# Performance work log

Hardware: AMD Instinct MI355X
Metric: run time of the kernel (lower is better)

The kernel has to match this reference:

```python
import jax, jax.numpy as jnp
import numpy as np

N = 32768      # nodes
DIN = 256      # in_channels (space dim; hyperbolic input has DIN+1 dims)
DOUT = 256     # out_channels
H = 8          # num_heads
K = 1.0        # Lorentz curvature manifold.k
P = 2          # power_k
EPS = 1e-6


def _lorentz(key, n, d):
    # random point on Lorentz manifold: time = sqrt(||space||^2 + k)
    s = jax.random.normal(key, (n, d), jnp.float32)
    t = jnp.sqrt(jnp.sum(s * s, -1, keepdims=True) + K)
    return jnp.concatenate([t, s], -1)


def setup_inputs() -> dict:
    key = jax.random.key(0)
    ks = jax.random.split(key, 8)
    sc = 0.02
    return {
        "query_input": _lorentz(ks[0], N, DIN),
        "source_input": _lorentz(ks[1], N, DIN),
        "Wq_w": jax.random.normal(ks[2], (H, DOUT, DIN + 1), jnp.float32) * sc,
        "Wq_b": jnp.zeros((H, DOUT), jnp.float32),
        "Wk_w": jax.random.normal(ks[3], (H, DOUT, DIN + 1), jnp.float32) * sc,
        "Wk_b": jnp.zeros((H, DOUT), jnp.float32),
        "Wv_w": jax.random.normal(ks[4], (H, DOUT, DIN + 1), jnp.float32) * sc,
        "Wv_b": jnp.zeros((H, DOUT), jnp.float32),
        "norm_scale": jnp.ones((), jnp.float32),
        "v_map_w": jax.random.normal(ks[5], (DOUT, DIN), jnp.float32) * sc,
        "v_map_b": jnp.zeros((DOUT,), jnp.float32),
        "final_w": jax.random.normal(ks[6], (DOUT, H * DOUT), jnp.float32) * sc,
        "final_b": jnp.zeros((DOUT,), jnp.float32),
    }


def _hyp_linear(x, W, b):
    # HypLinear for all heads at once. x: [N, Din+1], W: [H, Dout, Din+1], b: [H, Dout]
    xs = jnp.einsum('ni,hoi->nho', x, W) + b              # space part [N,H,Dout]
    xt = jnp.sqrt(jnp.sum(xs * xs, -1, keepdims=True) + K)  # Lorentz time
    return jnp.concatenate([xt, xs], -1)                  # [N,H,Dout+1]


def _fp(x, p=P):
    # fp(x) = ||x|| / ||x^p|| * x^p  (per-vector rescaled power map)
    norm_x = jnp.linalg.norm(x, axis=-1, keepdims=True)
    xp = x ** p
    norm_xp = jnp.linalg.norm(xp, axis=-1, keepdims=True)
    return norm_x / norm_xp * xp


def reference(query_input, source_input, Wq_w, Wq_b, Wk_w, Wk_b, Wv_w, Wv_b,
              norm_scale, v_map_w, v_map_b, final_w, final_b):
    q = _hyp_linear(query_input, Wq_w, Wq_b)    # [N,H,D+1]
    k = _hyp_linear(source_input, Wk_w, Wk_b)   # [N,H,D+1]
    v = _hyp_linear(source_input, Wv_w, Wv_b)   # [N,H,D+1]

    # linear_focus_attention: drop time dim
    qs, ks_, vs = q[..., 1:], k[..., 1:], v[..., 1:]     # [N,H,D]
    dscale = jnp.abs(norm_scale) + EPS
    phi_q = _fp((jax.nn.relu(qs) + EPS) / dscale)
    phi_k = _fp((jax.nn.relu(ks_) + EPS) / dscale)

    ktv = jnp.einsum('nhm,nhd->hmd', phi_k, vs)          # [H,D,D]
    numerator = jnp.einsum('nhm,hmd->nhd', phi_q, ktv)   # [N,H,D]
    denominator = jnp.einsum('nhd,hd->nh', phi_q, jnp.sum(phi_k, 0))[..., None]
    attn = numerator / (denominator + EPS)

    vss = vs @ v_map_w.T + v_map_b                       # v_map_mlp(v)
    attn = attn + vss

    # trans_heads_concat -> final_linear
    out = attn.reshape(N, H * DOUT) @ final_w.T + final_b  # [N,Dout]

    # lift back to Lorentz manifold
    t = jnp.sqrt(jnp.sum(out * out, -1, keepdims=True) + K)
    return jnp.concatenate([t, out], -1)                 # [N,Dout+1]
```

## Files before the change

kernel.cpp:

```cpp
#include <hip/hip_runtime.h>
#include <hip/hip_bf16.h>


#define EPSF 1e-6f

typedef __attribute__((ext_vector_type(8))) short bf16x8;
typedef __attribute__((ext_vector_type(8))) unsigned short u16x8;
typedef __attribute__((ext_vector_type(4))) float f32x4;
typedef float f32x4a __attribute__((ext_vector_type(4), aligned(4)));

__device__ __forceinline__ float b2f(unsigned short u) {
    union { unsigned int i; float f; } c;
    c.i = ((unsigned int)u) << 16;
    return c.f;
}
__device__ __forceinline__ unsigned short f2b(float f) {
    __hip_bfloat16 h = __float2bfloat16(f);
    union { __hip_bfloat16 h; unsigned short u; } c;
    c.h = h;
    return c.u;
}

__global__ void zero_kernel(float* __restrict__ p, int n) {
    int i = blockIdx.x * 256 + threadIdx.x;
    if (i < n) p[i] = 0.f;
}

__global__ __launch_bounds__(256) void wconv_kernel(
    const float* __restrict__ Wq, const float* __restrict__ Wk, const float* __restrict__ Wv,
    const float* __restrict__ Bq, const float* __restrict__ Bk, const float* __restrict__ Bv,
    unsigned short* __restrict__ Wbf, float* __restrict__ biasAll)
{
    const int t = threadIdx.x;
    const int b = blockIdx.x;
    if (b < 6144) {
        const int mat = b >> 11, lr = b & 2047;
        const float* Ws = (mat == 0 ? Wq : mat == 1 ? Wk : Wv) + (size_t)lr * 257;
        Wbf[(size_t)b * 288 + t] = f2b(Ws[t]);
        if (t < 32) {
            float v = (t == 0) ? Ws[256] : 0.f;
            Wbf[(size_t)b * 288 + 256 + t] = f2b(v);
        }
    } else {
        const int e = (b - 6144) * 256 + t;
        const int mat = e >> 11, r = e & 2047;
        biasAll[e] = (mat == 0 ? Bq : mat == 1 ? Bk : Bv)[r];
    }
}

__global__ __launch_bounds__(256) void w2g_kernel(
    const float* __restrict__ vmw,
    const float* __restrict__ fw,
    float* __restrict__ G32)
{
    const int t = threadIdx.x;
    const int h = blockIdx.x >> 3;
    const int i0 = (blockIdx.x & 7) * 32;

    __shared__ __align__(16) float xlds[16][40];
    __shared__ float wlds[256][17];

    float acc[32];
#pragma unroll
    for (int r = 0; r < 32; ++r) acc[r] = 0.f;

    const int ar = t >> 3;
    const int ak = (t & 7) * 2;
    const int wk = t & 15;
    const int wo = (t >> 4) * 16;

    for (int d0 = 0; d0 < 256; d0 += 16) {
        xlds[ak][ar]     = vmw[(size_t)(d0 + ak) * 256 + i0 + ar];
        xlds[ak + 1][ar] = vmw[(size_t)(d0 + ak + 1) * 256 + i0 + ar];
#pragma unroll
        for (int j = 0; j < 16; ++j)
            wlds[wo + j][wk] = fw[(size_t)(wo + j) * 2048 + h * 256 + d0 + wk];
        __syncthreads();
#pragma unroll
        for (int kk = 0; kk < 16; ++kk) {
            float bv = wlds[t][kk];
            const float4* xr = (const float4*)(&xlds[kk][0]);
#pragma unroll
            for (int g = 0; g < 8; ++g) {
                float4 xv = xr[g];
                acc[g * 4 + 0] = fmaf(xv.x, bv, acc[g * 4 + 0]);
                acc[g * 4 + 1] = fmaf(xv.y, bv, acc[g * 4 + 1]);
                acc[g * 4 + 2] = fmaf(xv.z, bv, acc[g * 4 + 2]);
                acc[g * 4 + 3] = fmaf(xv.w, bv, acc[g * 4 + 3]);
            }
        }
        __syncthreads();
    }
#pragma unroll
    for (int r = 0; r < 32; ++r)
        G32[(size_t)t * 2048 + h * 256 + i0 + r] = acc[r];
}

__global__ __launch_bounds__(256) void bias2_kernel(
    const float* __restrict__ vmb, const float* __restrict__ fw,
    const float* __restrict__ fb, const float* __restrict__ Bv,
    const float* __restrict__ G32, float* __restrict__ bias2)
{
    const int o = blockIdx.x;
    const int t = threadIdx.x;
    float s = 0.f, sb = 0.f;
#pragma unroll
    for (int i = 0; i < 8; ++i) {
        const int j = t + i * 256;
        s += fw[(size_t)o * 2048 + j];
        sb += Bv[j] * G32[(size_t)o * 2048 + j];
    }
    s = s * vmb[t] + sb;
#pragma unroll
    for (int off = 32; off > 0; off >>= 1) s += __shfl_down(s, off, 64);
    __shared__ float r4[4];
    if ((t & 63) == 0) r4[t >> 6] = s;
    __syncthreads();
    if (t == 0) bias2[o] = fb[o] + r4[0] + r4[1] + r4[2] + r4[3];
}

__global__ __launch_bounds__(256) void gm_kernel(
    const float* __restrict__ Wv, const float* __restrict__ G32,
    float* __restrict__ Mf32)
{
    __shared__ float Gt[64][33];
    __shared__ float Wt[32][33];
    const int t = threadIdx.x;
    const int o0 = blockIdx.x * 64, i0 = blockIdx.y * 32, k0 = blockIdx.z * 256;
    const int ii = t & 31, og = t >> 5;
    float acc[8] = {};
    for (int kk0 = k0; kk0 < k0 + 256; kk0 += 32) {
#pragma unroll
        for (int r = 0; r < 8; ++r) {
            const int e = t + r * 256;
            Gt[e >> 5][e & 31] = G32[(size_t)(o0 + (e >> 5)) * 2048 + kk0 + (e & 31)];
        }
#pragma unroll
        for (int r = 0; r < 4; ++r) {
            const int e = t + r * 256;
            const int kk = e >> 5, i = i0 + (e & 31);
            Wt[kk][e & 31] = (i < 257) ? Wv[(size_t)(kk0 + kk) * 257 + i] : 0.f;
        }
        __syncthreads();
#pragma unroll
        for (int kk = 0; kk < 32; ++kk) {
            float wv_ = Wt[kk][ii];
#pragma unroll
            for (int r = 0; r < 8; ++r)
                acc[r] = fmaf(Gt[og * 8 + r][kk], wv_, acc[r]);
        }
        __syncthreads();
    }
#pragma unroll
    for (int r = 0; r < 8; ++r)
        atomicAdd(&Mf32[(size_t)(o0 + og * 8 + r) * 288 + i0 + ii], acc[r]);
}

__global__ void gmcvt_kernel(const float* __restrict__ Mf32, unsigned short* __restrict__ Mbf) {
    const int i = blockIdx.x * 256 + threadIdx.x;
    Mbf[i] = f2b(Mf32[i]);
}

__global__ __launch_bounds__(256) void proj_mfma(
    const float* __restrict__ X,
    const unsigned short* __restrict__ Wbase,
    const float* __restrict__ biasBase,
    unsigned short* __restrict__ outT,
    int CH)
{
    __shared__ __align__(16) unsigned short smem[10240];
    __shared__ float rowx[128];
    unsigned short* lA = smem;
    unsigned short* lB = smem + 128 * 40;
    const int t = threadIdx.x;
    const int m0 = blockIdx.x * 128;
    const int c0 = blockIdx.y * 128;
    const int lane = t & 63, w = t >> 6;
    const int wm = (w >> 1) * 64, wn = (w & 1) * 64;
    const int l15 = lane & 15, q = lane >> 4;
    const int ar = t >> 2, akg = (t & 3) * 8;

    f32x4 acc[4][4] = {};
    const float* XA = X + (size_t)(m0 + ar) * 257 + akg;
    const unsigned short* WB = Wbase + (size_t)(c0 + ar) * 288 + akg;

    f32x4a cx[2][2];
    u16x8 cw[2];
#pragma unroll
    for (int qq = 0; qq < 2; ++qq) {
        cx[qq][0] = *(const f32x4a*)(XA + (size_t)qq * 64 * 257);
        cx[qq][1] = *(const f32x4a*)(XA + (size_t)qq * 64 * 257 + 4);
        cw[qq]    = *(const u16x8*)(WB + (size_t)qq * 64 * 288);
    }

    for (int ks = 0; ks < 8; ++ks) {
#pragma unroll
        for (int qq = 0; qq < 2; ++qq) {
            u16x8 pk;
            pk[0] = f2b(cx[qq][0][0]); pk[1] = f2b(cx[qq][0][1]);
            pk[2] = f2b(cx[qq][0][2]); pk[3] = f2b(cx[qq][0][3]);
            pk[4] = f2b(cx[qq][1][0]); pk[5] = f2b(cx[qq][1][1]);
            pk[6] = f2b(cx[qq][1][2]); pk[7] = f2b(cx[qq][1][3]);
            *(u16x8*)(&lA[(ar + qq * 64) * 40 + akg]) = pk;
            *(u16x8*)(&lB[(ar + qq * 64) * 40 + akg]) = cw[qq];
        }
        if (ks < 7) {
            const int k1 = (ks + 1) * 32;
#pragma unroll
            for (int qq = 0; qq < 2; ++qq) {
                cx[qq][0] = *(const f32x4a*)(XA + (size_t)qq * 64 * 257 + k1);
                cx[qq][1] = *(const f32x4a*)(XA + (size_t)qq * 64 * 257 + k1 + 4);
                cw[qq]    = *(const u16x8*)(WB + (size_t)qq * 64 * 288 + k1);
            }
        }
        __syncthreads();
        bf16x8 af[4], bfr[4];
#pragma unroll
        for (int i = 0; i < 4; ++i)
            af[i] = *(const bf16x8*)(&lA[(wm + i * 16 + l15) * 40 + q * 8]);
#pragma unroll
        for (int j = 0; j < 4; ++j)
            bfr[j] = *(const bf16x8*)(&lB[(wn + j * 16 + l15) * 40 + q * 8]);
#pragma unroll
        for (int i = 0; i < 4; ++i)
#pragma unroll
            for (int j = 0; j < 4; ++j)
                acc[i][j] = __builtin_amdgcn_mfma_f32_16x16x32_bf16(af[i], bfr[j], acc[i][j], 0, 0, 0);
        __syncthreads();
    }

    if (t < 128) rowx[t] = b2f(f2b(X[(size_t)(m0 + t) * 257 + 256]));
    __syncthreads();

#pragma unroll
    for (int j = 0; j < 4; ++j) {
        const int cg = c0 + wn + j * 16 + l15;
        const float w256 = b2f(Wbase[(size_t)cg * 288 + 256]);
        const float bias = biasBase[cg];
#pragma unroll
        for (int i = 0; i < 4; ++i)
#pragma unroll
            for (int r = 0; r < 4; ++r)
                acc[i][j][r] += rowx[wm + i * 16 + q * 4 + r] * w256 + bias;
    }

#pragma unroll
    for (int p = 0; p < 2; ++p) {
        __syncthreads();
        if ((w >> 1) == p) {
#pragma unroll
            for (int i = 0; i < 4; ++i)
#pragma unroll
                for (int j = 0; j < 4; ++j) {
                    const int cl = wn + j * 16 + l15;
#pragma unroll
                    for (int r2 = 0; r2 < 4; r2 += 2) {
                        const int nl = i * 16 + q * 4 + r2;
                        const unsigned int pk =
                            (unsigned int)f2b(acc[i][j][r2]) |
                            ((unsigned int)f2b(acc[i][j][r2 + 1]) << 16);
                        *(unsigned int*)(&smem[cl * 64 + (((nl >> 3) ^ (cl & 7)) << 3) + (nl & 7)]) = pk;
                    }
                }
        }
        __syncthreads();
#pragma unroll
        for (int k = 0; k < 4; ++k) {
            const int task = k * 256 + t;
            const int cl = task >> 3, nq = task & 7;
            *(u16x8*)(outT + (size_t)(c0 + cl) * CH + m0 + p * 64 + nq * 8) =
                *(const u16x8*)(&smem[cl * 64 + ((nq ^ (cl & 7)) << 3)]);
        }
    }
}

__global__ __launch_bounds__(256) void xm_mfma(
    const float* __restrict__ X,
    const unsigned short* __restrict__ Mbf,
    float* __restrict__ outp)
{
    __shared__ __align__(16) unsigned short smem[10240];
    __shared__ float rowx[128];
    unsigned short* lA = smem;
    unsigned short* lB = smem + 128 * 40;
    const int t = threadIdx.x;
    const int m0 = blockIdx.x * 128;
    const int c0 = blockIdx.y * 128;
    const int lane = t & 63, w = t >> 6;
    const int wm = (w >> 1) * 64, wn = (w & 1) * 64;
    const int l15 = lane & 15, q = lane >> 4;
    const int ar = t >> 2, akg = (t & 3) * 8;

    f32x4 acc[4][4] = {};
    const float* XA = X + (size_t)(m0 + ar) * 257 + akg;
    const unsigned short* WB = Mbf + (size_t)(c0 + ar) * 288 + akg;

    f32x4a cx[2][2];
    u16x8 cw[2];
#pragma unroll
    for (int qq = 0; qq < 2; ++qq) {
        cx[qq][0] = *(const f32x4a*)(XA + (size_t)qq * 64 * 257);
        cx[qq][1] = *(const f32x4a*)(XA + (size_t)qq * 64 * 257 + 4);
        cw[qq]    = *(const u16x8*)(WB + (size_t)qq * 64 * 288);
    }

    for (int ks = 0; ks < 8; ++ks) {
#pragma unroll
        for (int qq = 0; qq < 2; ++qq) {
            u16x8 pk;
            pk[0] = f2b(cx[qq][0][0]); pk[1] = f2b(cx[qq][0][1]);
            pk[2] = f2b(cx[qq][0][2]); pk[3] = f2b(cx[qq][0][3]);
            pk[4] = f2b(cx[qq][1][0]); pk[5] = f2b(cx[qq][1][1]);
            pk[6] = f2b(cx[qq][1][2]); pk[7] = f2b(cx[qq][1][3]);
            *(u16x8*)(&lA[(ar + qq * 64) * 40 + akg]) = pk;
            *(u16x8*)(&lB[(ar + qq * 64) * 40 + akg]) = cw[qq];
        }
        if (ks < 7) {
            const int k1 = (ks + 1) * 32;
#pragma unroll
            for (int qq = 0; qq < 2; ++qq) {
                cx[qq][0] = *(const f32x4a*)(XA + (size_t)qq * 64 * 257 + k1);
                cx[qq][1] = *(const f32x4a*)(XA + (size_t)qq * 64 * 257 + k1 + 4);
                cw[qq]    = *(const u16x8*)(WB + (size_t)qq * 64 * 288 + k1);
            }
        }
        __syncthreads();
        bf16x8 af[4], bfr[4];
#pragma unroll
        for (int i = 0; i < 4; ++i)
            af[i] = *(const bf16x8*)(&lA[(wm + i * 16 + l15) * 40 + q * 8]);
#pragma unroll
        for (int j = 0; j < 4; ++j)
            bfr[j] = *(const bf16x8*)(&lB[(wn + j * 16 + l15) * 40 + q * 8]);
#pragma unroll
        for (int i = 0; i < 4; ++i)
#pragma unroll
            for (int j = 0; j < 4; ++j)
                acc[i][j] = __builtin_amdgcn_mfma_f32_16x16x32_bf16(af[i], bfr[j], acc[i][j], 0, 0, 0);
        __syncthreads();
    }

    if (t < 128) rowx[t] = b2f(f2b(X[(size_t)(m0 + t) * 257 + 256]));
    __syncthreads();

#pragma unroll
    for (int j = 0; j < 4; ++j) {
        const int cg = c0 + wn + j * 16 + l15;
        const float w256 = b2f(Mbf[(size_t)cg * 288 + 256]);
#pragma unroll
        for (int i = 0; i < 4; ++i)
#pragma unroll
            for (int r = 0; r < 4; ++r) {
                const int n = m0 + wm + i * 16 + q * 4 + r;
                outp[(size_t)n * 257 + 1 + cg] =
                    acc[i][j][r] + rowx[wm + i * 16 + q * 4 + r] * w256;
            }
    }
}

__global__ __launch_bounds__(256) void proj_phi(
    const float* __restrict__ X,
    const unsigned short* __restrict__ Wbase,
    const float* __restrict__ biasBase,
    unsigned short* __restrict__ outbuf,
    const float* __restrict__ nsc,
    const float* __restrict__ colsum_in,
    float* __restrict__ colsum_rep,
    int mode, int CH)
{
    __shared__ __align__(16) unsigned short smem[16384];
    __shared__ float reds2[4][64];
    __shared__ float reds4[4][64];
    __shared__ float rowv[64];
    __shared__ float rowx[64];
    unsigned short* lA = smem;
    unsigned short* lB = smem + 64 * 40;

    const int t = threadIdx.x;
    const int m0 = blockIdx.x * 64;
    const int h  = blockIdx.y;
    const int lane = t & 63, w = t >> 6;
    const int wn = w * 64;
    const int l15 = lane & 15, q = lane >> 4;
    const int ar = t >> 2, akg = (t & 3) * 8;

    f32x4 acc[4][4] = {};
    const float* XA = X + (size_t)(m0 + ar) * 257 + akg;
    const unsigned short* WB = Wbase + (size_t)(h * 256 + ar) * 288 + akg;

    f32x4a cx0, cx1;
    u16x8 cw[4];
    cx0 = *(const f32x4a*)(XA);
    cx1 = *(const f32x4a*)(XA + 4);
#pragma unroll
    for (int qq = 0; qq < 4; ++qq)
        cw[qq] = *(const u16x8*)(WB + (size_t)qq * 64 * 288);

    for (int ks = 0; ks < 8; ++ks) {
        {
            u16x8 pk;
            pk[0] = f2b(cx0[0]); pk[1] = f2b(cx0[1]);
            pk[2] = f2b(cx0[2]); pk[3] = f2b(cx0[3]);
            pk[4] = f2b(cx1[0]); pk[5] = f2b(cx1[1]);
            pk[6] = f2b(cx1[2]); pk[7] = f2b(cx1[3]);
            *(u16x8*)(&lA[ar * 40 + akg]) = pk;
        }
#pragma unroll
        for (int qq = 0; qq < 4; ++qq)
            *(u16x8*)(&lB[(ar + qq * 64) * 40 + akg]) = cw[qq];
        if (ks < 7) {
            const int k1 = (ks + 1) * 32;
            cx0 = *(const f32x4a*)(XA + k1);
            cx1 = *(const f32x4a*)(XA + k1 + 4);
#pragma unroll
            for (int qq = 0; qq < 4; ++qq)
                cw[qq] = *(const u16x8*)(WB + (size_t)qq * 64 * 288 + k1);
        }
        __syncthreads();
        bf16x8 af[4], bfr[4];
#pragma unroll
        for (int i = 0; i < 4; ++i)
            af[i] = *(const bf16x8*)(&lA[(i * 16 + l15) * 40 + q * 8]);
#pragma unroll
        for (int j = 0; j < 4; ++j)
            bfr[j] = *(const bf16x8*)(&lB[(wn + j * 16 + l15) * 40 + q * 8]);
#pragma unroll
        for (int i = 0; i < 4; ++i)
#pragma unroll
            for (int j = 0; j < 4; ++j)
                acc[i][j] = __builtin_amdgcn_mfma_f32_16x16x32_bf16(af[i], bfr[j], acc[i][j], 0, 0, 0);
        __syncthreads();
    }

    if (t < 64) rowx[t] = b2f(f2b(X[(size_t)(m0 + t) * 257 + 256]));
    __syncthreads();

    {
        float w256[4];
#pragma unroll
        for (int j = 0; j < 4; ++j)
            w256[j] = b2f(Wbase[(size_t)(h * 256 + wn + j * 16 + l15) * 288 + 256]);
#pragma unroll
        for (int i = 0; i < 4; ++i)
#pragma unroll
            for (int r = 0; r < 4; ++r) {
                const float xv = rowx[i * 16 + q * 4 + r];
#pragma unroll
                for (int j = 0; j < 4; ++j)
                    acc[i][j][r] += xv * w256[j];
            }
    }

    const float c = fabsf(nsc[0]) + EPSF;
    float bias[4];
#pragma unroll
    for (int j = 0; j < 4; ++j) bias[j] = biasBase[h * 256 + wn + j * 16 + l15];

    float a2[4][4], a4[4][4];
#pragma unroll
    for (int i = 0; i < 4; ++i)
#pragma unroll
        for (int r = 0; r < 4; ++r) { a2[i][r] = 0.f; a4[i][r] = 0.f; }
#pragma unroll
    for (int i = 0; i < 4; ++i)
#pragma unroll
        for (int j = 0; j < 4; ++j)
#pragma unroll
            for (int r = 0; r < 4; ++r) {
                float uu = fmaxf(acc[i][j][r] + bias[j], 0.f) + EPSF;
                float q2 = uu * uu;
                acc[i][j][r] = q2;
                a2[i][r] += q2;
                a4[i][r] += q2 * q2;
            }
#pragma unroll
    for (int m = 1; m <= 8; m <<= 1) {
#pragma unroll
        for (int i = 0; i < 4; ++i)
#pragma unroll
            for (int r = 0; r < 4; ++r) {
                a2[i][r] += __shfl_xor(a2[i][r], m, 64);
                a4[i][r] += __shfl_xor(a4[i][r], m, 64);
            }
    }
    if (l15 == 0) {
#pragma unroll
        for (int i = 0; i < 4; ++i)
#pragma unroll
            for (int r = 0; r < 4; ++r) {
                reds2[w][i * 16 + q * 4 + r] = a2[i][r];
                reds4[w][i * 16 + q * 4 + r] = a4[i][r];
            }
    }
    __syncthreads();
    if (t < 64) {
        float s2t = reds2[0][t] + reds2[1][t] + reds2[2][t] + reds2[3][t];
        float s4t = reds4[0][t] + reds4[1][t] + reds4[2][t] + reds4[3][t];
        rowv[t] = sqrtf(s2t) / (c * sqrtf(s4t));
    }
    __syncthreads();
    float sc_[4][4];
#pragma unroll
    for (int i = 0; i < 4; ++i)
#pragma unroll
        for (int r = 0; r < 4; ++r) sc_[i][r] = rowv[i * 16 + q * 4 + r];

    if (mode == 0) {
        float colp[4];
#pragma unroll
        for (int j = 0; j < 4; ++j) colp[j] = 0.f;
#pragma unroll
        for (int i = 0; i < 4; ++i)
#pragma unroll
            for (int j = 0; j < 4; ++j)
#pragma unroll
                for (int r = 0; r < 4; ++r) {
                    float ph = acc[i][j][r] * sc_[i][r];
                    acc[i][j][r] = ph;
                    colp[j] += ph;
                }
#pragma unroll
        for (int i = 0; i < 4; ++i)
#pragma unroll
            for (int j = 0; j < 4; ++j) {
                const int cl = wn + j * 16 + l15;
#pragma unroll
                for (int r2 = 0; r2 < 4; r2 += 2) {
                    const int nl = i * 16 + q * 4 + r2;
                    const unsigned int pk =
                        (unsigned int)f2b(acc[i][j][r2]) |
                        ((unsigned int)f2b(acc[i][j][r2 + 1]) << 16);
                    *(unsigned int*)(&smem[cl * 64 + (((nl >> 3) ^ (cl & 7)) << 3) + (nl & 7)]) = pk;
                }
            }
        __syncthreads();
#pragma unroll
        for (int k = 0; k < 8; ++k) {
            const int task = k * 256 + t;
            const int cl = task >> 3, nq = task & 7;
            *(u16x8*)(outbuf + (size_t)(h * 256 + cl) * CH + m0 + nq * 8) =
                *(const u16x8*)(&smem[cl * 64 + ((nq ^ (cl & 7)) << 3)]);
        }
#pragma unroll
        for (int j = 0; j < 4; ++j) {
            colp[j] += __shfl_xor(colp[j], 16, 64);
            colp[j] += __shfl_xor(colp[j], 32, 64);
        }
        if (q == 0) {
            float* dst = colsum_rep + (size_t)(blockIdx.x & 7) * 2048;
#pragma unroll
            for (int j = 0; j < 4; ++j)
                atomicAdd(&dst[h * 256 + wn + j * 16 + l15], colp[j]);
        }
    } else {
        float cs[4];
#pragma unroll
        for (int j = 0; j < 4; ++j) cs[j] = colsum_in[h * 256 + wn + j * 16 + l15];
        float dp[4][4];
#pragma unroll
        for (int i = 0; i < 4; ++i)
#pragma unroll
            for (int r = 0; r < 4; ++r) dp[i][r] = 0.f;
#pragma unroll
        for (int i = 0; i < 4; ++i)
#pragma unroll
            for (int j = 0; j < 4; ++j)
#pragma unroll
                for (int r = 0; r < 4; ++r) {
                    float ph = acc[i][j][r] * sc_[i][r];
                    acc[i][j][r] = ph;
                    dp[i][r] += ph * cs[j];
                }
#pragma unroll
        for (int m = 1; m <= 8; m <<= 1) {
#pragma unroll
            for (int i = 0; i < 4; ++i)
#pragma unroll
                for (int r = 0; r < 4; ++r)
                    dp[i][r] += __shfl_xor(dp[i][r], m, 64);
        }
        if (l15 == 0) {
#pragma unroll
            for (int i = 0; i < 4; ++i)
#pragma unroll
                for (int r = 0; r < 4; ++r)
                    reds2[w][i * 16 + q * 4 + r] = dp[i][r];
        }
        __syncthreads();
        if (t < 64) {
            float dt = reds2[0][t] + reds2[1][t] + reds2[2][t] + reds2[3][t];
            rowv[t] = 1.f / (dt + EPSF);
        }
        __syncthreads();
#pragma unroll
        for (int i = 0; i < 4; ++i)
#pragma unroll
            for (int r = 0; r < 4; ++r) sc_[i][r] = rowv[i * 16 + q * 4 + r];
#pragma unroll
        for (int i = 0; i < 4; ++i)
#pragma unroll
            for (int j = 0; j < 4; ++j)
#pragma unroll
                for (int r = 0; r < 4; ++r) {
                    const int n = m0 + i * 16 + q * 4 + r;
                    outbuf[(size_t)n * 2048 + h * 256 + wn + j * 16 + l15] =
                        f2b(acc[i][j][r] * sc_[i][r]);
                }
    }
}

__global__ __launch_bounds__(256) void merge_colsum(
    const float* __restrict__ rep, float* __restrict__ out)
{
    const int cidx = blockIdx.x * 256 + threadIdx.x;
    float s = 0.f;
#pragma unroll
    for (int r = 0; r < 8; ++r) s += rep[(size_t)r * 2048 + cidx];
    out[cidx] = s;
}

__global__ __launch_bounds__(256) void ktv_mfma(
    const unsigned short* __restrict__ phiT,
    const unsigned short* __restrict__ vsT,
    float* __restrict__ ktv, int CH)
{
    __shared__ __align__(16) unsigned short lAT[128 * 64];
    __shared__ __align__(16) unsigned short lBT[128 * 64];
    const int t = threadIdx.x;
    const int h = blockIdx.y;
    const int split = blockIdx.x >> 2;
    const int tile = blockIdx.x & 3;
    const int m0 = (tile >> 1) * 128, d0 = (tile & 1) * 128;
    const int chh = h * 256;
    const int lane = t & 63, w = t >> 6;
    const int wm = (w >> 1) * 64, wn = (w & 1) * 64;
    const int l15 = lane & 15, q = lane >> 4;
    const int sl7 = l15 & 7;

    const int scg  = t >> 3;
    const int snq  = t & 7;
    const int sbase = scg * 64 + ((snq ^ (scg & 7)) << 3);

    f32x4 acc[4][4] = {};
    const int nb0 = split * 512;

    const unsigned short* pA = phiT + (size_t)(chh + m0 + scg) * CH + snq * 8;
    const unsigned short* pB = vsT  + (size_t)(chh + d0 + scg) * CH + snq * 8;

    u16x8 cA[4], cB[4], nA[4], nB[4];
#pragma unroll
    for (int k = 0; k < 4; ++k) {
        cA[k] = *(const u16x8*)(pA + (size_t)(k * 32) * CH + nb0);
        cB[k] = *(const u16x8*)(pB + (size_t)(k * 32) * CH + nb0);
    }

    for (int it = 0; it < 8; ++it) {
#pragma unroll
        for (int k = 0; k < 4; ++k) {
            *(u16x8*)(&lAT[k * 2048 + sbase]) = cA[k];
            *(u16x8*)(&lBT[k * 2048 + sbase]) = cB[k];
        }
        if (it < 7) {
            const int nb = nb0 + (it + 1) * 64;
#pragma unroll
            for (int k = 0; k < 4; ++k) {
                nA[k] = *(const u16x8*)(pA + (size_t)(k * 32) * CH + nb);
                nB[k] = *(const u16x8*)(pB + (size_t)(k * 32) * CH + nb);
            }
        }
        __syncthreads();
#pragma unroll
        for (int sub = 0; sub < 2; ++sub) {
            const int slot = ((sub * 4 + q) ^ sl7) << 3;
            bf16x8 af[4], bfr[4];
#pragma unroll
            for (int i = 0; i < 4; ++i)
                af[i] = *(const bf16x8*)(&lAT[(wm + i * 16 + l15) * 64 + slot]);
#pragma unroll
            for (int j = 0; j < 4; ++j)
                bfr[j] = *(const bf16x8*)(&lBT[(wn + j * 16 + l15) * 64 + slot]);
#pragma unroll
            for (int i = 0; i < 4; ++i)
#pragma unroll
                for (int j = 0; j < 4; ++j)
                    acc[i][j] = __builtin_amdgcn_mfma_f32_16x16x32_bf16(af[i], bfr[j], acc[i][j], 0, 0, 0);
        }
        __syncthreads();
        if (it < 7) {
#pragma unroll
            for (int k = 0; k < 4; ++k) { cA[k] = nA[k]; cB[k] = nB[k]; }
        }
    }
#pragma unroll
    for (int i = 0; i < 4; ++i)
#pragma unroll
        for (int j = 0; j < 4; ++j)
#pragma unroll
            for (int r = 0; r < 4; ++r) {
                const int m = m0 + wm + i * 16 + q * 4 + r;
                const int d = d0 + wn + j * 16 + l15;
                atomicAdd(&ktv[((size_t)chh + m) * 256 + d], acc[i][j][r]);
            }
}

__device__ __forceinline__ void fin_load(
    const unsigned short* __restrict__ Abuf, const unsigned short* __restrict__ W2T,
    int n0, int d0, int t, int k0,
    u16x8& A0, u16x8& A1, u16x8& B)
{
    {
        const int row = t >> 2, kg = (t & 3) * 8;
        A0 = *(const u16x8*)(Abuf + (size_t)(n0 + row) * 2048 + ((k0 + kg) & 2047));
    }
    {
        const int e = t + 256;
        const int row = e >> 2, kg = (e & 3) * 8;
        A1 = *(const u16x8*)(Abuf + (size_t)(n0 + row) * 2048 + ((k0 + kg) & 2047));
    }
    {
        const int row = t >> 2, kg = (t & 3) * 8;
        B = *(const u16x8*)(W2T + (size_t)(d0 + row) * 4096 + k0 + kg);
    }
}

__global__ __launch_bounds__(256) void final_mfma(
    const unsigned short* __restrict__ Abuf,
    const unsigned short* __restrict__ W2T,
    int kbeg, int kend,
    float* __restrict__ outp)
{
    __shared__ __align__(16) unsigned short lA[128 * 40];
    __shared__ __align__(16) unsigned short lB[64 * 40];
    const int t = threadIdx.x;
    const int n0 = blockIdx.x * 128;
    const int d0 = blockIdx.y * 64;
    const int khalf = (kend - kbeg) >> 1;
    const int kb = kbeg + blockIdx.z * khalf;
    const int ke = kb + khalf;
    const int lane = t & 63, w = t >> 6;
    const int wm = w * 32;
    const int l15 = lane & 15, q = lane >> 4;

    f32x4 acc[2][4] = {};
    u16x8 cA0, cA1, cB, nA0, nA1, nB;
    fin_load(Abuf, W2T, n0, d0, t, kb, cA0, cA1, cB);

    for (int k0 = kb; k0 < ke; k0 += 32) {
        {
            const int row = t >> 2, kg = (t & 3) * 8;
            *(u16x8*)(&lA[row * 40 + kg]) = cA0;
            *(u16x8*)(&lB[row * 40 + kg]) = cB;
        }
        {
            const int e = t + 256;
            const int row = e >> 2, kg = (e & 3) * 8;
            *(u16x8*)(&lA[row * 40 + kg]) = cA1;
        }
        if (k0 + 32 < ke)
            fin_load(Abuf, W2T, n0, d0, t, k0 + 32, nA0, nA1, nB);
        __syncthreads();
        bf16x8 af[2], bfr[4];
#pragma unroll
        for (int i = 0; i < 2; ++i)
            af[i] = *(const bf16x8*)(&lA[(wm + i * 16 + l15) * 40 + q * 8]);
#pragma unroll
        for (int j = 0; j < 4; ++j)
            bfr[j] = *(const bf16x8*)(&lB[(j * 16 + l15) * 40 + q * 8]);
#pragma unroll
        for (int i = 0; i < 2; ++i)
#pragma unroll
            for (int j = 0; j < 4; ++j)
                acc[i][j] = __builtin_amdgcn_mfma_f32_16x16x32_bf16(af[i], bfr[j], acc[i][j], 0, 0, 0);
        __syncthreads();
        if (k0 + 32 < ke) { cA0 = nA0; cA1 = nA1; cB = nB; }
    }
#pragma unroll
    for (int i = 0; i < 2; ++i)
#pragma unroll
        for (int j = 0; j < 4; ++j)
#pragma unroll
            for (int r = 0; r < 4; ++r) {
                const int n = n0 + wm + i * 16 + q * 4 + r;
                const int d = d0 + j * 16 + l15;
                atomicAdd(&outp[(size_t)n * 257 + 1 + d], acc[i][j][r]);
            }
}

__global__ __launch_bounds__(256) void w2u_kernel(
    const float* __restrict__ ktv,
    const float* __restrict__ fw,
    unsigned short* __restrict__ W2T)
{
    const int t = threadIdx.x;
    const int h = blockIdx.x >> 3;
    const int m0 = (blockIdx.x & 7) * 32;

    __shared__ __align__(16) float xlds[16][40];
    __shared__ float wlds[256][17];

    float acc[32];
#pragma unroll
    for (int r = 0; r < 32; ++r) acc[r] = 0.f;

    const int ar = t >> 3;
    const int ak = (t & 7) * 2;
    const int wk = t & 15;
    const int wo = (t >> 4) * 16;

    for (int d0 = 0; d0 < 256; d0 += 16) {
        {
            const float* src = ktv + (size_t)(h * 256 + m0 + ar) * 256 + d0 + ak;
            xlds[ak][ar]     = src[0];
            xlds[ak + 1][ar] = src[1];
        }
#pragma unroll
        for (int j = 0; j < 16; ++j)
            wlds[wo + j][wk] = fw[(size_t)(wo + j) * 2048 + h * 256 + d0 + wk];
        __syncthreads();
#pragma unroll
        for (int kk = 0; kk < 16; ++kk) {
            float bv = wlds[t][kk];
            const float4* xr = (const float4*)(&xlds[kk][0]);
#pragma unroll
            for (int g = 0; g < 8; ++g) {
                float4 xv = xr[g];
                acc[g * 4 + 0] = fmaf(xv.x, bv, acc[g * 4 + 0]);
                acc[g * 4 + 1] = fmaf(xv.y, bv, acc[g * 4 + 1]);
                acc[g * 4 + 2] = fmaf(xv.z, bv, acc[g * 4 + 2]);
                acc[g * 4 + 3] = fmaf(xv.w, bv, acc[g * 4 + 3]);
            }
        }
        __syncthreads();
    }
#pragma unroll
    for (int r = 0; r < 32; ++r)
        W2T[(size_t)t * 4096 + h * 256 + m0 + r] = f2b(acc[r]);
}

__global__ __launch_bounds__(256) void lift_kernel(
    const float* __restrict__ bias2, float* __restrict__ outp)
{
    const int t = threadIdx.x;
    const int lane = t & 63;
    const int w = t >> 6;
    const int n0 = blockIdx.x * 64 + w * 16;
    float b[4];
#pragma unroll
    for (int j = 0; j < 4; ++j) b[j] = bias2[lane + j * 64];
    for (int r = 0; r < 16; ++r) {
        float* row = outp + (size_t)(n0 + r) * 257;
        float v[4];
        float s = 0.f;
#pragma unroll
        for (int j = 0; j < 4; ++j) {
            v[j] = row[1 + lane + j * 64] + b[j];
            s = fmaf(v[j], v[j], s);
        }
#pragma unroll
        for (int off = 32; off > 0; off >>= 1) s += __shfl_down(s, off, 64);
#pragma unroll
        for (int j = 0; j < 4; ++j) row[1 + lane + j * 64] = v[j];
        if (lane == 0) row[0] = sqrtf(s + 1.0f);
    }
}

extern "C" void kernel_launch(void* const* d_in, const int* in_sizes, int n_in,
                              void* d_out, int out_size, void* d_ws, size_t ws_size,
                              hipStream_t stream)
{
    const float* xq  = (const float*)d_in[0];
    const float* xs  = (const float*)d_in[1];
    const float* Wq  = (const float*)d_in[2];
    const float* Bq  = (const float*)d_in[3];
    const float* Wk  = (const float*)d_in[4];
    const float* Bk  = (const float*)d_in[5];
    const float* Wv  = (const float*)d_in[6];
    const float* Bv  = (const float*)d_in[7];
    const float* nsc = (const float*)d_in[8];
    const float* vmw = (const float*)d_in[9];
    const float* vmb = (const float*)d_in[10];
    const float* fw  = (const float*)d_in[11];
    const float* fb  = (const float*)d_in[12];
    float* outp = (float*)d_out;

    char* ws = (char*)d_ws;
    float* ktv          = (float*)(ws + 0);
    float* colrep       = (float*)(ws + 2097152);
    float* Mf32         = (float*)(ws + 2162688);
    float* colsum       = (float*)(ws + 2457600);
    float* bias2        = (float*)(ws + 2465792);
    float* biasAll      = (float*)(ws + 2466816);
    unsigned short* W2T = (unsigned short*)(ws + 2491392);
    unsigned short* Wbf = (unsigned short*)(ws + 4588544);
    float* G32          = (float*)(ws + 8127488);
    unsigned short* Mbf = (unsigned short*)(ws + 10224640);
    const size_t fixedBytes = 10372096;

    int CH = 2048;
    if (ws_size >= fixedBytes + (size_t)8192 * 8192) CH = 8192;
    else if (ws_size >= fixedBytes + (size_t)4096 * 8192) CH = 4096;
    const int NCHK = 32768 / CH;
    unsigned short* phibuf = (unsigned short*)(ws + fixedBytes);
    unsigned short* vsT    = (unsigned short*)(ws + fixedBytes + (size_t)CH * 4096);

    zero_kernel<<<dim3(2400), 256, 0, stream>>>(ktv, 614400);
    wconv_kernel<<<dim3(6168), 256, 0, stream>>>(Wq, Wk, Wv, Bq, Bk, Bv, Wbf, biasAll);
    w2g_kernel<<<dim3(64), 256, 0, stream>>>(vmw, fw, G32);
    bias2_kernel<<<dim3(256), 256, 0, stream>>>(vmb, fw, fb, Bv, G32, bias2);
    gm_kernel<<<dim3(4, 9, 8), 256, 0, stream>>>(Wv, G32, Mf32);
    gmcvt_kernel<<<dim3(288), 256, 0, stream>>>(Mf32, Mbf);

    for (int c = 0; c < NCHK; ++c) {
        const float* xs_c = xs + (size_t)c * CH * 257;
        float* out_c = outp + (size_t)c * CH * 257;
        proj_phi<<<dim3(CH / 64, 8), 256, 0, stream>>>(
            xs_c, Wbf + (size_t)2048 * 288, biasAll + 2048, phibuf,
            nsc, nullptr, colrep, 0, CH);
        proj_mfma<<<dim3(CH / 128, 16), 256, 0, stream>>>(
            xs_c, Wbf + (size_t)4096 * 288, biasAll + 4096, vsT, CH);
        xm_mfma<<<dim3(CH / 128, 2), 256, 0, stream>>>(xs_c, Mbf, out_c);
        ktv_mfma<<<dim3((CH / 512) * 4, 8), 256, 0, stream>>>(phibuf, vsT, ktv, CH);
    }

    merge_colsum<<<dim3(8), 256, 0, stream>>>(colrep, colsum);
    w2u_kernel<<<dim3(64), 256, 0, stream>>>(ktv, fw, W2T);

    for (int c = 0; c < NCHK; ++c) {
        const float* xq_c = xq + (size_t)c * CH * 257;
        float* out_c = outp + (size_t)c * CH * 257;
        proj_phi<<<dim3(CH / 64, 8), 256, 0, stream>>>(
            xq_c, Wbf, biasAll, phibuf,
            nsc, colsum, nullptr, 1, CH);
        final_mfma<<<dim3(CH / 128, 4, 2), 256, 0, stream>>>(phibuf, W2T, 0, 2048, out_c);
    }

    lift_kernel<<<dim3(512), 256, 0, stream>>>(bias2, outp);
}
```

Before: 1.045 ms.

## Load MFMA operands directly from global into registers, dropping LDS staging

```diff
diff --git a/kernel.cpp b/kernel.cpp
--- a/kernel.cpp
+++ b/kernel.cpp
@@ -19,6 +19,13 @@
     union { __hip_bfloat16 h; unsigned short u; } c;
     c.h = h;
     return c.u;
+}
+__device__ __forceinline__ bf16x8 cvt8(f32x4a a, f32x4a b) {
+    u16x8 r;
+    r[0] = f2b(a[0]); r[1] = f2b(a[1]); r[2] = f2b(a[2]); r[3] = f2b(a[3]);
+    r[4] = f2b(b[0]); r[5] = f2b(b[1]); r[6] = f2b(b[2]); r[7] = f2b(b[3]);
+    union { u16x8 u; bf16x8 s; } c; c.u = r;
+    return c.s;
 }
 
 __global__ void zero_kernel(float* __restrict__ p, int n) {
@@ -161,6 +168,7 @@
     Mbf[i] = f2b(Mf32[i]);
 }
 
+
 __global__ __launch_bounds__(256) void proj_mfma(
     const float* __restrict__ X,
     const unsigned short* __restrict__ Wbase,
@@ -168,68 +176,62 @@
     unsigned short* __restrict__ outT,
     int CH)
 {
-    __shared__ __align__(16) unsigned short smem[10240];
-    __shared__ float rowx[128];
-    unsigned short* lA = smem;
-    unsigned short* lB = smem + 128 * 40;
-    const int t = threadIdx.x;
-    const int m0 = blockIdx.x * 128;
-    const int c0 = blockIdx.y * 128;
+    __shared__ __align__(16) unsigned short smem[16384];
+    __shared__ float rowx[64];
+    const int t = threadIdx.x;
+    const int m0 = blockIdx.x * 64;
+    const int c0 = blockIdx.y * 256;
     const int lane = t & 63, w = t >> 6;
-    const int wm = (w >> 1) * 64, wn = (w & 1) * 64;
+    const int wn = w * 64;
     const int l15 = lane & 15, q = lane >> 4;
-    const int ar = t >> 2, akg = (t & 3) * 8;
+
+    const float* xp = X + (size_t)(m0 + l15) * 257 + q * 8;
+    const unsigned short* wp = Wbase + (size_t)(c0 + wn + l15) * 288 + q * 8;
 
     f32x4 acc[4][4] = {};
-    const float* XA = X + (size_t)(m0 + ar) * 257 + akg;
-    const unsigned short* WB = Wbase + (size_t)(c0 + ar) * 288 + akg;
-
-    f32x4a cx[2][2];
-    u16x8 cw[2];
-#pragma unroll
-    for (int qq = 0; qq < 2; ++qq) {
-        cx[qq][0] = *(const f32x4a*)(XA + (size_t)qq * 64 * 257);
-        cx[qq][1] = *(const f32x4a*)(XA + (size_t)qq * 64 * 257 + 4);
-        cw[qq]    = *(const u16x8*)(WB + (size_t)qq * 64 * 288);
-    }
+    bf16x8 af[4], bw[4];
+    f32x4a xr[4][2];
+    bf16x8 wr[4];
+
+#pragma unroll
+    for (int i = 0; i < 4; ++i) {
+        xr[i][0] = *(const f32x4a*)(xp + (size_t)i * 16 * 257);
+        xr[i][1] = *(const f32x4a*)(xp + (size_t)i * 16 * 257 + 4);
+    }
+#pragma unroll
+    for (int j = 0; j < 4; ++j)
+        wr[j] = *(const bf16x8*)(wp + (size_t)j * 16 * 288);
+#pragma unroll
+    for (int i = 0; i < 4; ++i) af[i] = cvt8(xr[i][0], xr[i][1]);
+#pragma unroll
+    for (int j = 0; j < 4; ++j) bw[j] = wr[j];
 
     for (int ks = 0; ks < 8; ++ks) {
-#pragma unroll
-        for (int qq = 0; qq < 2; ++qq) {
-            u16x8 pk;
-            pk[0] = f2b(cx[qq][0][0]); pk[1] = f2b(cx[qq][0][1]);
-            pk[2] = f2b(cx[qq][0][2]); pk[3] = f2b(cx[qq][0][3]);
-            pk[4] = f2b(cx[qq][1][0]); pk[5] = f2b(cx[qq][1][1]);
-            pk[6] = f2b(cx[qq][1][2]); pk[7] = f2b(cx[qq][1][3]);
-            *(u16x8*)(&lA[(ar + qq * 64) * 40 + akg]) = pk;
-            *(u16x8*)(&lB[(ar + qq * 64) * 40 + akg]) = cw[qq];
-        }
         if (ks < 7) {
             const int k1 = (ks + 1) * 32;
 #pragma unroll
-            for (int qq = 0; qq < 2; ++qq) {
-                cx[qq][0] = *(const f32x4a*)(XA + (size_t)qq * 64 * 257 + k1);
-                cx[qq][1] = *(const f32x4a*)(XA + (size_t)qq * 64 * 257 + k1 + 4);
-                cw[qq]    = *(const u16x8*)(WB + (size_t)qq * 64 * 288 + k1);
-            }
-        }
-        __syncthreads();
-        bf16x8 af[4], bfr[4];
-#pragma unroll
-        for (int i = 0; i < 4; ++i)
-            af[i] = *(const bf16x8*)(&lA[(wm + i * 16 + l15) * 40 + q * 8]);
-#pragma unroll
-        for (int j = 0; j < 4; ++j)
-            bfr[j] = *(const bf16x8*)(&lB[(wn + j * 16 + l15) * 40 + q * 8]);
-#pragma unroll
-        for (int i = 0; i < 4; ++i)
-#pragma unroll
-            for (int j = 0; j < 4; ++j)
-                acc[i][j] = __builtin_amdgcn_mfma_f32_16x16x32_bf16(af[i], bfr[j], acc[i][j], 0, 0, 0);
-        __syncthreads();
-    }
-
-    if (t < 128) rowx[t] = b2f(f2b(X[(size_t)(m0 + t) * 257 + 256]));
+            for (int i = 0; i < 4; ++i) {
+                xr[i][0] = *(const f32x4a*)(xp + (size_t)i * 16 * 257 + k1);
+                xr[i][1] = *(const f32x4a*)(xp + (size_t)i * 16 * 257 + k1 + 4);
+            }
+#pragma unroll
+            for (int j = 0; j < 4; ++j)
+                wr[j] = *(const bf16x8*)(wp + (size_t)j * 16 * 288 + k1);
+        }
+#pragma unroll
+        for (int i = 0; i < 4; ++i)
+#pragma unroll
+            for (int j = 0; j < 4; ++j)
+                acc[i][j] = __builtin_amdgcn_mfma_f32_16x16x32_bf16(af[i], bw[j], acc[i][j], 0, 0, 0);
+        if (ks < 7) {
+#pragma unroll
+            for (int i = 0; i < 4; ++i) af[i] = cvt8(xr[i][0], xr[i][1]);
+#pragma unroll
+            for (int j = 0; j < 4; ++j) bw[j] = wr[j];
+        }
+    }
+
+    if (t < 64) rowx[t] = b2f(f2b(X[(size_t)(m0 + t) * 257 + 256]));
     __syncthreads();
 
 #pragma unroll
@@ -241,36 +243,30 @@
         for (int i = 0; i < 4; ++i)
 #pragma unroll
             for (int r = 0; r < 4; ++r)
-                acc[i][j][r] += rowx[wm + i * 16 + q * 4 + r] * w256 + bias;
-    }
-
-#pragma unroll
-    for (int p = 0; p < 2; ++p) {
-        __syncthreads();
-        if ((w >> 1) == p) {
-#pragma unroll
-            for (int i = 0; i < 4; ++i)
-#pragma unroll
-                for (int j = 0; j < 4; ++j) {
-                    const int cl = wn + j * 16 + l15;
-#pragma unroll
-                    for (int r2 = 0; r2 < 4; r2 += 2) {
-                        const int nl = i * 16 + q * 4 + r2;
-                        const unsigned int pk =
-                            (unsigned int)f2b(acc[i][j][r2]) |
-                            ((unsigned int)f2b(acc[i][j][r2 + 1]) << 16);
-                        *(unsigned int*)(&smem[cl * 64 + (((nl >> 3) ^ (cl & 7)) << 3) + (nl & 7)]) = pk;
-                    }
-                }
-        }
-        __syncthreads();
-#pragma unroll
-        for (int k = 0; k < 4; ++k) {
-            const int task = k * 256 + t;
-            const int cl = task >> 3, nq = task & 7;
-            *(u16x8*)(outT + (size_t)(c0 + cl) * CH + m0 + p * 64 + nq * 8) =
-                *(const u16x8*)(&smem[cl * 64 + ((nq ^ (cl & 7)) << 3)]);
-        }
+                acc[i][j][r] += rowx[i * 16 + q * 4 + r] * w256 + bias;
+    }
+
+#pragma unroll
+    for (int i = 0; i < 4; ++i)
+#pragma unroll
+        for (int j = 0; j < 4; ++j) {
+            const int cl = wn + j * 16 + l15;
+#pragma unroll
+            for (int r2 = 0; r2 < 4; r2 += 2) {
+                const int nl = i * 16 + q * 4 + r2;
+                const unsigned int pk =
+                    (unsigned int)f2b(acc[i][j][r2]) |
+                    ((unsigned int)f2b(acc[i][j][r2 + 1]) << 16);
+                *(unsigned int*)(&smem[cl * 64 + (((nl >> 3) ^ (cl & 7)) << 3) + (nl & 7)]) = pk;
+            }
+        }
+    __syncthreads();
+#pragma unroll
+    for (int k = 0; k < 8; ++k) {
+        const int task = k * 256 + t;
+        const int cl = task >> 3, nq = task & 7;
+        *(u16x8*)(outT + (size_t)(c0 + cl) * CH + m0 + nq * 8) =
+            *(const u16x8*)(&smem[cl * 64 + ((nq ^ (cl & 7)) << 3)]);
     }
 }
 
@@ -279,81 +275,73 @@
     const unsigned short* __restrict__ Mbf,
     float* __restrict__ outp)
 {
-    __shared__ __align__(16) unsigned short smem[10240];
-    __shared__ float rowx[128];
-    unsigned short* lA = smem;
-    unsigned short* lB = smem + 128 * 40;
-    const int t = threadIdx.x;
-    const int m0 = blockIdx.x * 128;
-    const int c0 = blockIdx.y * 128;
+    __shared__ float rowx[64];
+    const int t = threadIdx.x;
+    const int m0 = blockIdx.x * 64;
     const int lane = t & 63, w = t >> 6;
-    const int wm = (w >> 1) * 64, wn = (w & 1) * 64;
+    const int wn = w * 64;
     const int l15 = lane & 15, q = lane >> 4;
-    const int ar = t >> 2, akg = (t & 3) * 8;
+
+    const float* xp = X + (size_t)(m0 + l15) * 257 + q * 8;
+    const unsigned short* wp = Mbf + (size_t)(wn + l15) * 288 + q * 8;
 
     f32x4 acc[4][4] = {};
-    const float* XA = X + (size_t)(m0 + ar) * 257 + akg;
-    const unsigned short* WB = Mbf + (size_t)(c0 + ar) * 288 + akg;
-
-    f32x4a cx[2][2];
-    u16x8 cw[2];
-#pragma unroll
-    for (int qq = 0; qq < 2; ++qq) {
-        cx[qq][0] = *(const f32x4a*)(XA + (size_t)qq * 64 * 257);
-        cx[qq][1] = *(const f32x4a*)(XA + (size_t)qq * 64 * 257 + 4);
-        cw[qq]    = *(const u16x8*)(WB + (size_t)qq * 64 * 288);
-    }
+    bf16x8 af[4], bw[4];
+    f32x4a xr[4][2];
+    bf16x8 wr[4];
+
+#pragma unroll
+    for (int i = 0; i < 4; ++i) {
+        xr[i][0] = *(const f32x4a*)(xp + (size_t)i * 16 * 257);
+        xr[i][1] = *(const f32x4a*)(xp + (size_t)i * 16 * 257 + 4);
+    }
+#pragma unroll
+    for (int j = 0; j < 4; ++j)
+        wr[j] = *(const bf16x8*)(wp + (size_t)j * 16 * 288);
+#pragma unroll
+    for (int i = 0; i < 4; ++i) af[i] = cvt8(xr[i][0], xr[i][1]);
+#pragma unroll
+    for (int j = 0; j < 4; ++j) bw[j] = wr[j];
 
     for (int ks = 0; ks < 8; ++ks) {
-#pragma unroll
-        for (int qq = 0; qq < 2; ++qq) {
-            u16x8 pk;
-            pk[0] = f2b(cx[qq][0][0]); pk[1] = f2b(cx[qq][0][1]);
-            pk[2] = f2b(cx[qq][0][2]); pk[3] = f2b(cx[qq][0][3]);
-            pk[4] = f2b(cx[qq][1][0]); pk[5] = f2b(cx[qq][1][1]);
-            pk[6] = f2b(cx[qq][1][2]); pk[7] = f2b(cx[qq][1][3]);
-            *(u16x8*)(&lA[(ar + qq * 64) * 40 + akg]) = pk;
-            *(u16x8*)(&lB[(ar + qq * 64) * 40 + akg]) = cw[qq];
-        }
         if (ks < 7) {
             const int k1 = (ks + 1) * 32;
 #pragma unroll
-            for (int qq = 0; qq < 2; ++qq) {
-                cx[qq][0] = *(const f32x4a*)(XA + (size_t)qq * 64 * 257 + k1);
-                cx[qq][1] = *(const f32x4a*)(XA + (size_t)qq * 64 * 257 + k1 + 4);
-                cw[qq]    = *(const u16x8*)(WB + (size_t)qq * 64 * 288 + k1);
-            }
-        }
-        __syncthreads();
-        bf16x8 af[4], bfr[4];
-#pragma unroll
-        for (int i = 0; i < 4; ++i)
-            af[i] = *(const bf16x8*)(&lA[(wm + i * 16 + l15) * 40 + q * 8]);
-#pragma unroll
-        for (int j = 0; j < 4; ++j)
-            bfr[j] = *(const bf16x8*)(&lB[(wn + j * 16 + l15) * 40 + q * 8]);
-#pragma unroll
-        for (int i = 0; i < 4; ++i)
-#pragma unroll
-            for (int j = 0; j < 4; ++j)
-                acc[i][j] = __builtin_amdgcn_mfma_f32_16x16x32_bf16(af[i], bfr[j], acc[i][j], 0, 0, 0);
-        __syncthreads();
-    }
-
-    if (t < 128) rowx[t] = b2f(f2b(X[(size_t)(m0 + t) * 257 + 256]));
+            for (int i = 0; i < 4; ++i) {
+                xr[i][0] = *(const f32x4a*)(xp + (size_t)i * 16 * 257 + k1);
+                xr[i][1] = *(const f32x4a*)(xp + (size_t)i * 16 * 257 + k1 + 4);
+            }
+#pragma unroll
+            for (int j = 0; j < 4; ++j)
+                wr[j] = *(const bf16x8*)(wp + (size_t)j * 16 * 288 + k1);
+        }
+#pragma unroll
+        for (int i = 0; i < 4; ++i)
+#pragma unroll
+            for (int j = 0; j < 4; ++j)
+                acc[i][j] = __builtin_amdgcn_mfma_f32_16x16x32_bf16(af[i], bw[j], acc[i][j], 0, 0, 0);
+        if (ks < 7) {
+#pragma unroll
+            for (int i = 0; i < 4; ++i) af[i] = cvt8(xr[i][0], xr[i][1]);
+#pragma unroll
+            for (int j = 0; j < 4; ++j) bw[j] = wr[j];
+        }
+    }
+
+    if (t < 64) rowx[t] = b2f(f2b(X[(size_t)(m0 + t) * 257 + 256]));
     __syncthreads();
 
 #pragma unroll
     for (int j = 0; j < 4; ++j) {
-        const int cg = c0 + wn + j * 16 + l15;
+        const int cg = wn + j * 16 + l15;
         const float w256 = b2f(Mbf[(size_t)cg * 288 + 256]);
 #pragma unroll
         for (int i = 0; i < 4; ++i)
 #pragma unroll
             for (int r = 0; r < 4; ++r) {
-                const int n = m0 + wm + i * 16 + q * 4 + r;
+                const int n = m0 + i * 16 + q * 4 + r;
                 outp[(size_t)n * 257 + 1 + cg] =
-                    acc[i][j][r] + rowx[wm + i * 16 + q * 4 + r] * w256;
+                    acc[i][j][r] + rowx[i * 16 + q * 4 + r] * w256;
             }
     }
 }
@@ -373,8 +361,6 @@
     __shared__ float reds4[4][64];
     __shared__ float rowv[64];
     __shared__ float rowx[64];
-    unsigned short* lA = smem;
-    unsigned short* lB = smem + 64 * 40;
 
     const int t = threadIdx.x;
     const int m0 = blockIdx.x * 64;
@@ -382,54 +368,51 @@
     const int lane = t & 63, w = t >> 6;
     const int wn = w * 64;
     const int l15 = lane & 15, q = lane >> 4;
-    const int ar = t >> 2, akg = (t & 3) * 8;
+
+    const float* xp = X + (size_t)(m0 + l15) * 257 + q * 8;
+    const unsigned short* wp = Wbase + (size_t)(h * 256 + wn + l15) * 288 + q * 8;
 
     f32x4 acc[4][4] = {};
-    const float* XA = X + (size_t)(m0 + ar) * 257 + akg;
-    const unsigned short* WB = Wbase + (size_t)(h * 256 + ar) * 288 + akg;
-
-    f32x4a cx0, cx1;
-    u16x8 cw[4];
-    cx0 = *(const f32x4a*)(XA);
-    cx1 = *(const f32x4a*)(XA + 4);
-#pragma unroll
-    for (int qq = 0; qq < 4; ++qq)
-        cw[qq] = *(const u16x8*)(WB + (size_t)qq * 64 * 288);
+    bf16x8 af[4], bw[4];
+    f32x4a xr[4][2];
+    bf16x8 wr[4];
+
+#pragma unroll
+    for (int i = 0; i < 4; ++i) {
+        xr[i][0] = *(const f32x4a*)(xp + (size_t)i * 16 * 257);
+        xr[i][1] = *(const f32x4a*)(xp + (size_t)i * 16 * 257 + 4);
+    }
+#pragma unroll
+    for (int j = 0; j < 4; ++j)
+        wr[j] = *(const bf16x8*)(wp + (size_t)j * 16 * 288);
+#pragma unroll
+    for (int i = 0; i < 4; ++i) af[i] = cvt8(xr[i][0], xr[i][1]);
+#pragma unroll
+    for (int j = 0; j < 4; ++j) bw[j] = wr[j];
 
     for (int ks = 0; ks < 8; ++ks) {
-        {
-            u16x8 pk;
-            pk[0] = f2b(cx0[0]); pk[1] = f2b(cx0[1]);
-            pk[2] = f2b(cx0[2]); pk[3] = f2b(cx0[3]);
-            pk[4] = f2b(cx1[0]); pk[5] = f2b(cx1[1]);
-            pk[6] = f2b(cx1[2]); pk[7] = f2b(cx1[3]);
-            *(u16x8*)(&lA[ar * 40 + akg]) = pk;
-        }
-#pragma unroll
-        for (int qq = 0; qq < 4; ++qq)
-            *(u16x8*)(&lB[(ar + qq * 64) * 40 + akg]) = cw[qq];
         if (ks < 7) {
             const int k1 = (ks + 1) * 32;
-            cx0 = *(const f32x4a*)(XA + k1);
-            cx1 = *(const f32x4a*)(XA + k1 + 4);
-#pragma unroll
-            for (int qq = 0; qq < 4; ++qq)
-                cw[qq] = *(const u16x8*)(WB + (size_t)qq * 64 * 288 + k1);
-        }
-        __syncthreads();
-        bf16x8 af[4], bfr[4];
-#pragma unroll
-        for (int i = 0; i < 4; ++i)
-            af[i] = *(const bf16x8*)(&lA[(i * 16 + l15) * 40 + q * 8]);
-#pragma unroll
-        for (int j = 0; j < 4; ++j)
-            bfr[j] = *(const bf16x8*)(&lB[(wn + j * 16 + l15) * 40 + q * 8]);
-#pragma unroll
-        for (int i = 0; i < 4; ++i)
-#pragma unroll
-            for (int j = 0; j < 4; ++j)
-                acc[i][j] = __builtin_amdgcn_mfma_f32_16x16x32_bf16(af[i], bfr[j], acc[i][j], 0, 0, 0);
-        __syncthreads();
+#pragma unroll
+            for (int i = 0; i < 4; ++i) {
+                xr[i][0] = *(const f32x4a*)(xp + (size_t)i * 16 * 257 + k1);
+                xr[i][1] = *(const f32x4a*)(xp + (size_t)i * 16 * 257 + k1 + 4);
+            }
+#pragma unroll
+            for (int j = 0; j < 4; ++j)
+                wr[j] = *(const bf16x8*)(wp + (size_t)j * 16 * 288 + k1);
+        }
+#pragma unroll
+        for (int i = 0; i < 4; ++i)
+#pragma unroll
+            for (int j = 0; j < 4; ++j)
+                acc[i][j] = __builtin_amdgcn_mfma_f32_16x16x32_bf16(af[i], bw[j], acc[i][j], 0, 0, 0);
+        if (ks < 7) {
+#pragma unroll
+            for (int i = 0; i < 4; ++i) af[i] = cvt8(xr[i][0], xr[i][1]);
+#pragma unroll
+            for (int j = 0; j < 4; ++j) bw[j] = wr[j];
+        }
     }
 
     if (t < 64) rowx[t] = b2f(f2b(X[(size_t)(m0 + t) * 257 + 256]));
@@ -916,9 +899,9 @@
         proj_phi<<<dim3(CH / 64, 8), 256, 0, stream>>>(
             xs_c, Wbf + (size_t)2048 * 288, biasAll + 2048, phibuf,
             nsc, nullptr, colrep, 0, CH);
-        proj_mfma<<<dim3(CH / 128, 16), 256, 0, stream>>>(
+        proj_mfma<<<dim3(CH / 64, 8), 256, 0, stream>>>(
             xs_c, Wbf + (size_t)4096 * 288, biasAll + 4096, vsT, CH);
-        xm_mfma<<<dim3(CH / 128, 2), 256, 0, stream>>>(xs_c, Mbf, out_c);
+        xm_mfma<<<dim3(CH / 64), 256, 0, stream>>>(xs_c, Mbf, out_c);
         ktv_mfma<<<dim3((CH / 512) * 4, 8), 256, 0, stream>>>(phibuf, vsT, ktv, CH);
     }
 
```

Result: slower. 1.282 ms (+22.6%).

## Store transposed phi_k and v tiles in contiguous node stripes; stage row outputs through LDS

Applied to the files above, without the earlier changes.

```diff
diff --git a/kernel.cpp b/kernel.cpp
--- a/kernel.cpp
+++ b/kernel.cpp
@@ -8,6 +8,8 @@
 typedef __attribute__((ext_vector_type(8))) unsigned short u16x8;
 typedef __attribute__((ext_vector_type(4))) float f32x4;
 typedef float f32x4a __attribute__((ext_vector_type(4), aligned(4)));
+
+#define STRIPE 131072
 
 __device__ __forceinline__ float b2f(unsigned short u) {
     union { unsigned int i; float f; } c;
@@ -268,7 +270,8 @@
         for (int k = 0; k < 4; ++k) {
             const int task = k * 256 + t;
             const int cl = task >> 3, nq = task & 7;
-            *(u16x8*)(outT + (size_t)(c0 + cl) * CH + m0 + p * 64 + nq * 8) =
+            *(u16x8*)(outT + (size_t)(blockIdx.x * 2 + p) * STRIPE +
+                      (size_t)(c0 + cl) * 64 + nq * 8) =
                 *(const u16x8*)(&smem[cl * 64 + ((nq ^ (cl & 7)) << 3)]);
         }
     }
@@ -368,7 +371,7 @@
     float* __restrict__ colsum_rep,
     int mode, int CH)
 {
-    __shared__ __align__(16) unsigned short smem[16384];
+    __shared__ __align__(16) unsigned short smem[16896];
     __shared__ float reds2[4][64];
     __shared__ float reds4[4][64];
     __shared__ float rowv[64];
@@ -538,7 +541,8 @@
         for (int k = 0; k < 8; ++k) {
             const int task = k * 256 + t;
             const int cl = task >> 3, nq = task & 7;
-            *(u16x8*)(outbuf + (size_t)(h * 256 + cl) * CH + m0 + nq * 8) =
+            *(u16x8*)(outbuf + (size_t)blockIdx.x * STRIPE +
+                      (size_t)(h * 256 + cl) * 64 + nq * 8) =
                 *(const u16x8*)(&smem[cl * 64 + ((nq ^ (cl & 7)) << 3)]);
         }
 #pragma unroll
@@ -599,13 +603,22 @@
 #pragma unroll
         for (int i = 0; i < 4; ++i)
 #pragma unroll
-            for (int j = 0; j < 4; ++j)
+            for (int j = 0; j < 4; ++j) {
+                const int cl = wn + j * 16 + l15;
 #pragma unroll
                 for (int r = 0; r < 4; ++r) {
-                    const int n = m0 + i * 16 + q * 4 + r;
-                    outbuf[(size_t)n * 2048 + h * 256 + wn + j * 16 + l15] =
-                        f2b(acc[i][j][r] * sc_[i][r]);
+                    const int nl = i * 16 + q * 4 + r;
+                    smem[nl * 264 + cl] = f2b(acc[i][j][r] * sc_[i][r]);
                 }
+            }
+        __syncthreads();
+#pragma unroll
+        for (int k = 0; k < 8; ++k) {
+            const int task = k * 256 + t;
+            const int rowl = task >> 5, ck = (task & 31) * 8;
+            *(u16x8*)(outbuf + (size_t)(m0 + rowl) * 2048 + h * 256 + ck) =
+                *(const u16x8*)(&smem[rowl * 264 + ck]);
+        }
     }
 }
 
@@ -642,16 +655,16 @@
     const int sbase = scg * 64 + ((snq ^ (scg & 7)) << 3);
 
     f32x4 acc[4][4] = {};
-    const int nb0 = split * 512;
-
-    const unsigned short* pA = phiT + (size_t)(chh + m0 + scg) * CH + snq * 8;
-    const unsigned short* pB = vsT  + (size_t)(chh + d0 + scg) * CH + snq * 8;
+    const int st0 = split * 8;
+
+    const unsigned short* pA = phiT + (size_t)(chh + m0 + scg) * 64 + snq * 8;
+    const unsigned short* pB = vsT  + (size_t)(chh + d0 + scg) * 64 + snq * 8;
 
     u16x8 cA[4], cB[4], nA[4], nB[4];
 #pragma unroll
     for (int k = 0; k < 4; ++k) {
-        cA[k] = *(const u16x8*)(pA + (size_t)(k * 32) * CH + nb0);
-        cB[k] = *(const u16x8*)(pB + (size_t)(k * 32) * CH + nb0);
+        cA[k] = *(const u16x8*)(pA + (size_t)st0 * STRIPE + k * 2048);
+        cB[k] = *(const u16x8*)(pB + (size_t)st0 * STRIPE + k * 2048);
     }
 
     for (int it = 0; it < 8; ++it) {
@@ -661,11 +674,11 @@
             *(u16x8*)(&lBT[k * 2048 + sbase]) = cB[k];
         }
         if (it < 7) {
-            const int nb = nb0 + (it + 1) * 64;
+            const size_t so = (size_t)(st0 + it + 1) * STRIPE;
 #pragma unroll
             for (int k = 0; k < 4; ++k) {
-                nA[k] = *(const u16x8*)(pA + (size_t)(k * 32) * CH + nb);
-                nB[k] = *(const u16x8*)(pB + (size_t)(k * 32) * CH + nb);
+                nA[k] = *(const u16x8*)(pA + so + k * 2048);
+                nB[k] = *(const u16x8*)(pB + so + k * 2048);
             }
         }
         __syncthreads();
```

Result: no change. 1.055 ms (+0.9%).
